# Optimization experiments

Measured on AMD Instinct MI355X. Metric: run time of the kernel, lower is better.

The kernel has to match this reference:

```python
import jax, jax.numpy as jnp
import numpy as np

B, T, F = 32, 4096, 512
H = 512

def setup_inputs() -> dict:
    key = jax.random.key(0)
    k1, k2, k3, k4, k5 = jax.random.split(key, 5)
    enc = jax.random.normal(k1, (B, T, F), dtype=jnp.float32)
    dec = jax.random.normal(k2, (B, F), dtype=jnp.float32)
    # Dense kernels (no bias), scaled like Glorot-ish init
    W1 = jax.random.normal(k3, (F, H), dtype=jnp.float32) / np.sqrt(F)
    W2 = jax.random.normal(k4, (F, H), dtype=jnp.float32) / np.sqrt(F)
    V = jax.random.normal(k5, (H, 1), dtype=jnp.float32) / np.sqrt(H)
    return {"encoder_outputs": enc, "dec_output": dec, "W1": W1, "W2": W2, "V": V}

def reference(encoder_outputs, dec_output, W1, W2, V):
    # Bahdanau additive attention, fully vectorized over time_steps
    # (the original runs this step-by-step via K.rnn; state is unchanged,
    # so the computation is embarrassingly parallel over t).
    w1_e = jnp.einsum('btf,fh->bth', encoder_outputs, W1)   # [B,T,H]
    w2_d = jnp.einsum('bf,fh->bh', dec_output, W2)          # [B,H]
    scores = jnp.einsum('bth,h->bt', jnp.tanh(w1_e + w2_d[:, None, :]), V[:, 0])  # [B,T]
    return jax.nn.softmax(scores, axis=1)
```

## Files before the change

kernel.cpp:

```cpp
#include <hip/hip_runtime.h>
#include <hip/hip_bf16.h>

#define B_ 32
#define T_ 4096
#define F_ 512
#define H_ 512

typedef float floatx4 __attribute__((ext_vector_type(4)));
typedef short short8 __attribute__((ext_vector_type(8)));

__device__ __forceinline__ unsigned pack2_bf16(float a, float b) {
  unsigned ua = __float_as_uint(a);
  unsigned ub = __float_as_uint(b);
  ua = (ua + 0x7FFFu + ((ua >> 16) & 1u)) >> 16;
  ub = (ub + 0x7FFFu + ((ub >> 16) & 1u)) & 0xFFFF0000u;
  return ua | ub;
}

__device__ __forceinline__ unsigned short f2bf16(float a) {
  unsigned ua = __float_as_uint(a);
  return (unsigned short)((ua + 0x7FFFu + ((ua >> 16) & 1u)) >> 16);
}

__device__ __forceinline__ float tanh_fast(float x) {
  float e = __expf(2.0f * x);
  return 1.0f - __fdividef(2.0f, e + 1.0f);
}

__device__ __forceinline__ void async_load16(const void* g, void* l) {
  __builtin_amdgcn_global_load_lds(
      (const __attribute__((address_space(1))) void*)g,
      (__attribute__((address_space(3))) void*)l, 16, 0, 0);
}

__global__ void prep_w1t(const float* __restrict__ W1, unsigned short* __restrict__ W1T) {
  __shared__ float tile[32][33];
  const int tx = threadIdx.x, ty = threadIdx.y;
  const int f = blockIdx.y * 32 + ty;
  const int h = blockIdx.x * 32 + tx;
  tile[ty][tx] = W1[f * H_ + h];
  __syncthreads();
  const int ho = blockIdx.x * 32 + ty;
  const int fo = blockIdx.y * 32 + tx;
  W1T[ho * F_ + fo] = f2bf16(tile[tx][ty]);
}

__global__ __launch_bounds__(128) void prep_w2d(const float* __restrict__ dec,
                                                const float* __restrict__ W2,
                                                float* __restrict__ w2d) {
  const int b = blockIdx.x;
  const int h = blockIdx.y * 128 + threadIdx.x;
  float s0 = 0.f, s1 = 0.f, s2 = 0.f, s3 = 0.f;
  for (int f = 0; f < F_; f += 4) {
    s0 += dec[b * F_ + f + 0] * W2[(f + 0) * H_ + h];
    s1 += dec[b * F_ + f + 1] * W2[(f + 1) * H_ + h];
    s2 += dec[b * F_ + f + 2] * W2[(f + 2) * H_ + h];
    s3 += dec[b * F_ + f + 3] * W2[(f + 3) * H_ + h];
  }
  w2d[b * H_ + h] = (s0 + s1) + (s2 + s3);
}

__global__ __launch_bounds__(256, 3) void fused_score(
    const float* __restrict__ enc, const unsigned short* __restrict__ W1T,
    const float* __restrict__ w2d, const float* __restrict__ V,
    float* __restrict__ scores) {
  __shared__ __align__(16) unsigned short As[2][128 * 40];
  __shared__ __align__(16) unsigned short Bs[2][128 * 32];

  const int tid = threadIdx.x;
  const int bid = blockIdx.x;
  const int xcd = bid & 7;
  const int ii = bid >> 3;
  const int n_blk = ii & 3;
  const int m_blk = xcd + ((ii >> 2) << 3);
  const int lane = tid & 63;
  const int wave = tid >> 6;
  const int wm = wave >> 1;
  const int wn = wave & 1;
  const int quad = lane >> 4;
  const int l16 = lane & 15;

  const int arow = tid >> 2;
  const int acol = (tid & 3) * 8;
  const float* aptr = enc + (size_t)(m_blk * 128 + arow) * F_ + acol;

  const int nb0 = wave * 32;
  const int bl_n = lane >> 2;
  const int bl_c = (lane & 3) ^ (bl_n & 3);
  const unsigned short* bsrc0 =
      W1T + (size_t)(n_blk * 128 + nb0 + bl_n) * F_ + bl_c * 8;
  const unsigned short* bsrc1 = bsrc0 + 16 * F_;

  floatx4 acc[4][4];
#pragma unroll
  for (int i = 0; i < 4; i++)
#pragma unroll
    for (int j = 0; j < 4; j++) acc[i][j] = (floatx4){0.f, 0.f, 0.f, 0.f};

  float4 a_pre[4];

#pragma unroll
  for (int rr = 0; rr < 2; ++rr) {
    a_pre[rr * 2 + 0] = *(const float4*)(aptr + rr * 64 * F_ + 0);
    a_pre[rr * 2 + 1] = *(const float4*)(aptr + rr * 64 * F_ + 4);
  }
#pragma unroll
  for (int rr = 0; rr < 2; ++rr) {
    uint4 pk;
    pk.x = pack2_bf16(a_pre[rr * 2].x, a_pre[rr * 2].y);
    pk.y = pack2_bf16(a_pre[rr * 2].z, a_pre[rr * 2].w);
    pk.z = pack2_bf16(a_pre[rr * 2 + 1].x, a_pre[rr * 2 + 1].y);
    pk.w = pack2_bf16(a_pre[rr * 2 + 1].z, a_pre[rr * 2 + 1].w);
    *(uint4*)&As[0][(arow + rr * 64) * 40 + acol] = pk;
  }
  async_load16(bsrc0, &Bs[0][nb0 * 32]);
  async_load16(bsrc1, &Bs[0][(nb0 + 16) * 32]);
  __syncthreads();

  for (int ks = 0; ks < 16; ++ks) {
    const int cur = ks & 1;
    const int nxt = cur ^ 1;

    if (ks < 15) {
      const int k1 = (ks + 1) * 32;
#pragma unroll
      for (int rr = 0; rr < 2; ++rr) {
        a_pre[rr * 2 + 0] = *(const float4*)(aptr + rr * 64 * F_ + k1);
        a_pre[rr * 2 + 1] = *(const float4*)(aptr + rr * 64 * F_ + k1 + 4);
      }
      async_load16(bsrc0 + k1, &Bs[nxt][nb0 * 32]);
      async_load16(bsrc1 + k1, &Bs[nxt][(nb0 + 16) * 32]);
    }

    short8 af[4], bfr[4];
#pragma unroll
    for (int i = 0; i < 4; i++)
      af[i] = *(const short8*)&As[cur][(wm * 64 + i * 16 + l16) * 40 + quad * 8];
#pragma unroll
    for (int j = 0; j < 4; j++)
      bfr[j] = *(const short8*)&Bs[cur][(wn * 64 + j * 16 + l16) * 32 +
                                        ((quad ^ (l16 & 3)) * 8)];
#pragma unroll
    for (int i = 0; i < 4; i++)
#pragma unroll
      for (int j = 0; j < 4; j++)
        acc[i][j] = __builtin_amdgcn_mfma_f32_16x16x32_bf16(af[i], bfr[j], acc[i][j], 0, 0, 0);

    if (ks < 15) {
#pragma unroll
      for (int rr = 0; rr < 2; ++rr) {
        uint4 pk;
        pk.x = pack2_bf16(a_pre[rr * 2].x, a_pre[rr * 2].y);
        pk.y = pack2_bf16(a_pre[rr * 2].z, a_pre[rr * 2].w);
        pk.z = pack2_bf16(a_pre[rr * 2 + 1].x, a_pre[rr * 2 + 1].y);
        pk.w = pack2_bf16(a_pre[rr * 2 + 1].z, a_pre[rr * 2 + 1].w);
        *(uint4*)&As[nxt][(arow + rr * 64) * 40 + acol] = pk;
      }
    }
    __syncthreads();
  }

  const int b = m_blk >> 5;
  float w2v[4], vv[4];
#pragma unroll
  for (int j = 0; j < 4; j++) {
    const int h = n_blk * 128 + wn * 64 + j * 16 + l16;
    w2v[j] = w2d[b * H_ + h];
    vv[j] = V[h];
  }
  float rs[4][4];
#pragma unroll
  for (int i = 0; i < 4; i++)
#pragma unroll
    for (int r = 0; r < 4; r++) {
      float s = 0.f;
#pragma unroll
      for (int j = 0; j < 4; j++) s += tanh_fast(acc[i][j][r] + w2v[j]) * vv[j];
      rs[i][r] = s;
    }
#pragma unroll
  for (int i = 0; i < 4; i++)
#pragma unroll
    for (int r = 0; r < 4; r++) {
      float s = rs[i][r];
      s += __shfl_xor(s, 1, 16);
      s += __shfl_xor(s, 2, 16);
      s += __shfl_xor(s, 4, 16);
      s += __shfl_xor(s, 8, 16);
      rs[i][r] = s;
    }
  if (l16 == 0) {
#pragma unroll
    for (int i = 0; i < 4; i++)
#pragma unroll
      for (int r = 0; r < 4; r++)
        atomicAdd(&scores[m_blk * 128 + wm * 64 + i * 16 + quad * 4 + r], rs[i][r]);
  }
}

__global__ __launch_bounds__(256) void softmax_rows(const float* __restrict__ scores,
                                                    float* __restrict__ out) {
  const int b = blockIdx.x;
  const int tid = threadIdx.x;
  const int wave = tid >> 6;
  __shared__ float red[4];
  float v[16];
  float mx = -1e30f;
#pragma unroll
  for (int i = 0; i < 16; i++) {
    v[i] = scores[b * T_ + i * 256 + tid];
    mx = fmaxf(mx, v[i]);
  }
#pragma unroll
  for (int o = 32; o > 0; o >>= 1) mx = fmaxf(mx, __shfl_xor(mx, o, 64));
  if ((tid & 63) == 0) red[wave] = mx;
  __syncthreads();
  mx = fmaxf(fmaxf(red[0], red[1]), fmaxf(red[2], red[3]));
  __syncthreads();
  float sum = 0.f;
#pragma unroll
  for (int i = 0; i < 16; i++) {
    v[i] = __expf(v[i] - mx);
    sum += v[i];
  }
#pragma unroll
  for (int o = 32; o > 0; o >>= 1) sum += __shfl_xor(sum, o, 64);
  if ((tid & 63) == 0) red[wave] = sum;
  __syncthreads();
  sum = (red[0] + red[1]) + (red[2] + red[3]);
  const float inv = 1.0f / sum;
#pragma unroll
  for (int i = 0; i < 16; i++) out[b * T_ + i * 256 + tid] = v[i] * inv;
}

extern "C" void kernel_launch(void* const* d_in, const int* in_sizes, int n_in,
                              void* d_out, int out_size, void* d_ws, size_t ws_size,
                              hipStream_t stream) {
  const float* enc = (const float*)d_in[0];
  const float* dec = (const float*)d_in[1];
  const float* W1 = (const float*)d_in[2];
  const float* W2 = (const float*)d_in[3];
  const float* V = (const float*)d_in[4];
  float* out = (float*)d_out;

  char* ws = (char*)d_ws;
  float* scores = (float*)ws;
  unsigned short* W1T = (unsigned short*)(ws + 524288);
  float* w2d = (float*)(ws + 1048576);

  (void)in_sizes; (void)n_in; (void)out_size; (void)ws_size;

  hipMemsetAsync(scores, 0, B_ * T_ * sizeof(float), stream);
  prep_w1t<<<dim3(16, 16), dim3(32, 32), 0, stream>>>(W1, W1T);
  prep_w2d<<<dim3(32, 4), dim3(128), 0, stream>>>(dec, W2, w2d);
  fused_score<<<dim3(4096), dim3(256), 0, stream>>>(enc, W1T, w2d, V, scores);
  softmax_rows<<<dim3(32), dim3(256), 0, stream>>>(scores, out);
}
```

Baseline: 477.2 us.

## Drop LDS staging in score GEMM and load MFMA fragments directly from global

The fused score kernel no longer stages encoder and W1T tiles through shared memory. Each wave now loads its MFMA operand fragments straight from global memory into registers, using a two-stage register double buffer, and converts fp32 to bf16 in registers. This removes the LDS writes, reads and per-step barriers, and launch bounds drop to 2 blocks per CU to make room for the extra registers. The two prep kernels are also merged into one launch. In exchange, every wave re-reads the A and B fragments from global or L2 with less cross-wave reuse, and occupancy falls.

```diff
diff --git a/kernel.cpp b/kernel.cpp
--- a/kernel.cpp
+++ b/kernel.cpp
@@ -9,14 +9,6 @@
 typedef float floatx4 __attribute__((ext_vector_type(4)));
 typedef short short8 __attribute__((ext_vector_type(8)));
 
-__device__ __forceinline__ unsigned pack2_bf16(float a, float b) {
-  unsigned ua = __float_as_uint(a);
-  unsigned ub = __float_as_uint(b);
-  ua = (ua + 0x7FFFu + ((ua >> 16) & 1u)) >> 16;
-  ub = (ub + 0x7FFFu + ((ub >> 16) & 1u)) & 0xFFFF0000u;
-  return ua | ub;
-}
-
 __device__ __forceinline__ unsigned short f2bf16(float a) {
   unsigned ua = __float_as_uint(a);
   return (unsigned short)((ua + 0x7FFFu + ((ua >> 16) & 1u)) >> 16);
@@ -27,46 +19,54 @@
   return 1.0f - __fdividef(2.0f, e + 1.0f);
 }
 
-__device__ __forceinline__ void async_load16(const void* g, void* l) {
-  __builtin_amdgcn_global_load_lds(
-      (const __attribute__((address_space(1))) void*)g,
-      (__attribute__((address_space(3))) void*)l, 16, 0, 0);
-}
-
-__global__ void prep_w1t(const float* __restrict__ W1, unsigned short* __restrict__ W1T) {
+__device__ __forceinline__ short8 cvt8(float4 lo, float4 hi) {
+  union { short8 s8; __hip_bfloat16 h[8]; } u;
+  u.h[0] = __float2bfloat16(lo.x);
+  u.h[1] = __float2bfloat16(lo.y);
+  u.h[2] = __float2bfloat16(lo.z);
+  u.h[3] = __float2bfloat16(lo.w);
+  u.h[4] = __float2bfloat16(hi.x);
+  u.h[5] = __float2bfloat16(hi.y);
+  u.h[6] = __float2bfloat16(hi.z);
+  u.h[7] = __float2bfloat16(hi.w);
+  return u.s8;
+}
+
+__global__ __launch_bounds__(1024) void prep_all(const float* __restrict__ W1,
+                                                 unsigned short* __restrict__ W1T,
+                                                 const float* __restrict__ dec,
+                                                 const float* __restrict__ W2,
+                                                 float* __restrict__ w2d) {
   __shared__ float tile[32][33];
-  const int tx = threadIdx.x, ty = threadIdx.y;
-  const int f = blockIdx.y * 32 + ty;
-  const int h = blockIdx.x * 32 + tx;
-  tile[ty][tx] = W1[f * H_ + h];
-  __syncthreads();
-  const int ho = blockIdx.x * 32 + ty;
-  const int fo = blockIdx.y * 32 + tx;
-  W1T[ho * F_ + fo] = f2bf16(tile[tx][ty]);
-}
-
-__global__ __launch_bounds__(128) void prep_w2d(const float* __restrict__ dec,
-                                                const float* __restrict__ W2,
-                                                float* __restrict__ w2d) {
-  const int b = blockIdx.x;
-  const int h = blockIdx.y * 128 + threadIdx.x;
-  float s0 = 0.f, s1 = 0.f, s2 = 0.f, s3 = 0.f;
-  for (int f = 0; f < F_; f += 4) {
-    s0 += dec[b * F_ + f + 0] * W2[(f + 0) * H_ + h];
-    s1 += dec[b * F_ + f + 1] * W2[(f + 1) * H_ + h];
-    s2 += dec[b * F_ + f + 2] * W2[(f + 2) * H_ + h];
-    s3 += dec[b * F_ + f + 3] * W2[(f + 3) * H_ + h];
-  }
-  w2d[b * H_ + h] = (s0 + s1) + (s2 + s3);
-}
-
-__global__ __launch_bounds__(256, 3) void fused_score(
+  if (blockIdx.x < 256) {
+    const int tx = threadIdx.x & 31, ty = threadIdx.x >> 5;
+    const int bx = blockIdx.x & 15, by = blockIdx.x >> 4;
+    const int f = by * 32 + ty;
+    const int h = bx * 32 + tx;
+    tile[ty][tx] = W1[f * H_ + h];
+    __syncthreads();
+    const int ho = bx * 32 + ty;
+    const int fo = by * 32 + tx;
+    W1T[ho * F_ + fo] = f2bf16(tile[tx][ty]);
+  } else {
+    const int g = (blockIdx.x - 256) * 1024 + threadIdx.x;
+    const int b = g >> 9;
+    const int h = g & 511;
+    float s0 = 0.f, s1 = 0.f, s2 = 0.f, s3 = 0.f;
+    for (int f = 0; f < F_; f += 4) {
+      s0 += dec[b * F_ + f + 0] * W2[(f + 0) * H_ + h];
+      s1 += dec[b * F_ + f + 1] * W2[(f + 1) * H_ + h];
+      s2 += dec[b * F_ + f + 2] * W2[(f + 2) * H_ + h];
+      s3 += dec[b * F_ + f + 3] * W2[(f + 3) * H_ + h];
+    }
+    w2d[b * H_ + h] = (s0 + s1) + (s2 + s3);
+  }
+}
+
+__global__ __launch_bounds__(256, 2) void fused_score(
     const float* __restrict__ enc, const unsigned short* __restrict__ W1T,
     const float* __restrict__ w2d, const float* __restrict__ V,
     float* __restrict__ scores) {
-  __shared__ __align__(16) unsigned short As[2][128 * 40];
-  __shared__ __align__(16) unsigned short Bs[2][128 * 32];
-
   const int tid = threadIdx.x;
   const int bid = blockIdx.x;
   const int xcd = bid & 7;
@@ -80,16 +80,14 @@
   const int quad = lane >> 4;
   const int l16 = lane & 15;
 
-  const int arow = tid >> 2;
-  const int acol = (tid & 3) * 8;
-  const float* aptr = enc + (size_t)(m_blk * 128 + arow) * F_ + acol;
-
-  const int nb0 = wave * 32;
-  const int bl_n = lane >> 2;
-  const int bl_c = (lane & 3) ^ (bl_n & 3);
-  const unsigned short* bsrc0 =
-      W1T + (size_t)(n_blk * 128 + nb0 + bl_n) * F_ + bl_c * 8;
-  const unsigned short* bsrc1 = bsrc0 + 16 * F_;
+  const float* ap[4];
+  const unsigned short* bp[4];
+#pragma unroll
+  for (int i = 0; i < 4; i++)
+    ap[i] = enc + (size_t)(m_blk * 128 + wm * 64 + i * 16 + l16) * F_ + quad * 8;
+#pragma unroll
+  for (int j = 0; j < 4; j++)
+    bp[j] = W1T + (size_t)(n_blk * 128 + wn * 64 + j * 16 + l16) * F_ + quad * 8;
 
   floatx4 acc[4][4];
 #pragma unroll
@@ -97,68 +95,40 @@
 #pragma unroll
     for (int j = 0; j < 4; j++) acc[i][j] = (floatx4){0.f, 0.f, 0.f, 0.f};
 
-  float4 a_pre[4];
-
-#pragma unroll
-  for (int rr = 0; rr < 2; ++rr) {
-    a_pre[rr * 2 + 0] = *(const float4*)(aptr + rr * 64 * F_ + 0);
-    a_pre[rr * 2 + 1] = *(const float4*)(aptr + rr * 64 * F_ + 4);
-  }
-#pragma unroll
-  for (int rr = 0; rr < 2; ++rr) {
-    uint4 pk;
-    pk.x = pack2_bf16(a_pre[rr * 2].x, a_pre[rr * 2].y);
-    pk.y = pack2_bf16(a_pre[rr * 2].z, a_pre[rr * 2].w);
-    pk.z = pack2_bf16(a_pre[rr * 2 + 1].x, a_pre[rr * 2 + 1].y);
-    pk.w = pack2_bf16(a_pre[rr * 2 + 1].z, a_pre[rr * 2 + 1].w);
-    *(uint4*)&As[0][(arow + rr * 64) * 40 + acol] = pk;
-  }
-  async_load16(bsrc0, &Bs[0][nb0 * 32]);
-  async_load16(bsrc1, &Bs[0][(nb0 + 16) * 32]);
-  __syncthreads();
-
-  for (int ks = 0; ks < 16; ++ks) {
-    const int cur = ks & 1;
-    const int nxt = cur ^ 1;
-
-    if (ks < 15) {
-      const int k1 = (ks + 1) * 32;
-#pragma unroll
-      for (int rr = 0; rr < 2; ++rr) {
-        a_pre[rr * 2 + 0] = *(const float4*)(aptr + rr * 64 * F_ + k1);
-        a_pre[rr * 2 + 1] = *(const float4*)(aptr + rr * 64 * F_ + k1 + 4);
-      }
-      async_load16(bsrc0 + k1, &Bs[nxt][nb0 * 32]);
-      async_load16(bsrc1 + k1, &Bs[nxt][(nb0 + 16) * 32]);
-    }
-
-    short8 af[4], bfr[4];
-#pragma unroll
-    for (int i = 0; i < 4; i++)
-      af[i] = *(const short8*)&As[cur][(wm * 64 + i * 16 + l16) * 40 + quad * 8];
-#pragma unroll
-    for (int j = 0; j < 4; j++)
-      bfr[j] = *(const short8*)&Bs[cur][(wn * 64 + j * 16 + l16) * 32 +
-                                        ((quad ^ (l16 & 3)) * 8)];
-#pragma unroll
-    for (int i = 0; i < 4; i++)
-#pragma unroll
-      for (int j = 0; j < 4; j++)
-        acc[i][j] = __builtin_amdgcn_mfma_f32_16x16x32_bf16(af[i], bfr[j], acc[i][j], 0, 0, 0);
-
-    if (ks < 15) {
-#pragma unroll
-      for (int rr = 0; rr < 2; ++rr) {
-        uint4 pk;
-        pk.x = pack2_bf16(a_pre[rr * 2].x, a_pre[rr * 2].y);
-        pk.y = pack2_bf16(a_pre[rr * 2].z, a_pre[rr * 2].w);
-        pk.z = pack2_bf16(a_pre[rr * 2 + 1].x, a_pre[rr * 2 + 1].y);
-        pk.w = pack2_bf16(a_pre[rr * 2 + 1].z, a_pre[rr * 2 + 1].w);
-        *(uint4*)&As[nxt][(arow + rr * 64) * 40 + acol] = pk;
-      }
-    }
-    __syncthreads();
-  }
+#define ISSUE(RA, RB, K)                                     \
+  do {                                                       \
+    _Pragma("unroll") for (int i_ = 0; i_ < 4; i_++) {       \
+      RA[2 * i_ + 0] = *(const float4*)(ap[i_] + (K));       \
+      RA[2 * i_ + 1] = *(const float4*)(ap[i_] + (K) + 4);   \
+    }                                                        \
+    _Pragma("unroll") for (int j_ = 0; j_ < 4; j_++)         \
+      RB[j_] = *(const short8*)(bp[j_] + (K));               \
+  } while (0)
+
+#define COMPUTE(RA, RB)                                               \
+  do {                                                                \
+    _Pragma("unroll") for (int i_ = 0; i_ < 4; i_++) {                \
+      short8 af_ = cvt8(RA[2 * i_ + 0], RA[2 * i_ + 1]);              \
+      _Pragma("unroll") for (int j_ = 0; j_ < 4; j_++)                \
+        acc[i_][j_] = __builtin_amdgcn_mfma_f32_16x16x32_bf16(        \
+            af_, RB[j_], acc[i_][j_], 0, 0, 0);                       \
+    }                                                                 \
+  } while (0)
+
+  float4 raA[8], raB[8];
+  short8 rbA[4], rbB[4];
+
+  ISSUE(raA, rbA, 0);
+  ISSUE(raB, rbB, 32);
+#pragma unroll
+  for (int ks = 0; ks < 16; ks += 2) {
+    COMPUTE(raA, rbA);
+    if (ks + 2 < 16) ISSUE(raA, rbA, (ks + 2) * 32);
+    COMPUTE(raB, rbB);
+    if (ks + 3 < 16) ISSUE(raB, rbB, (ks + 3) * 32);
+  }
+#undef ISSUE
+#undef COMPUTE
 
   const int b = m_blk >> 5;
   float w2v[4], vv[4];
@@ -251,8 +221,7 @@
   (void)in_sizes; (void)n_in; (void)out_size; (void)ws_size;
 
   hipMemsetAsync(scores, 0, B_ * T_ * sizeof(float), stream);
-  prep_w1t<<<dim3(16, 16), dim3(32, 32), 0, stream>>>(W1, W1T);
-  prep_w2d<<<dim3(32, 4), dim3(128), 0, stream>>>(dec, W2, w2d);
+  prep_all<<<dim3(272), dim3(1024), 0, stream>>>(W1, W1T, dec, W2, w2d);
   fused_score<<<dim3(4096), dim3(256), 0, stream>>>(enc, W1T, w2d, V, scores);
   softmax_rows<<<dim3(32), dim3(256), 0, stream>>>(scores, out);
 }
```

Result: slower. 700.7 us (+46.8%).
